# Kernel optimization log

Hardware: AMD Instinct MI355X
Metric: run time of the kernel (lower is better)

Reference implementation:

```python
import jax, jax.numpy as jnp
import numpy as np

STEPS, K, NEW_PTS, GDIM, HDIM = 10, 64, 1152, 256, 128


def setup_inputs() -> dict:
    key = jax.random.key(0)
    ks = jax.random.split(key, 24)
    def w(k, shape):
        return jax.random.normal(k, shape, dtype=jnp.float32) * 0.02
    inp = {
        'points': jax.random.normal(ks[0], (4, 4096, 3), dtype=jnp.float32),
        'gt': jax.random.normal(ks[1], (4, 4096, 3), dtype=jnp.float32),
        # PointNet encoder: 3->64->128->256 (stored [in,out])
        'enc_w1': w(ks[2], (3, 64)),   'enc_b1': jnp.zeros((64,), jnp.float32),
        'enc_w2': w(ks[3], (64, 128)), 'enc_b2': jnp.zeros((128,), jnp.float32),
        'enc_w3': w(ks[4], (128, GDIM)), 'enc_b3': jnp.zeros((GDIM,), jnp.float32),
        # Attention MLP: (3+256+128)->128->1
        'att_w1': w(ks[5], (3 + GDIM + HDIM, 128)), 'att_b1': jnp.zeros((128,), jnp.float32),
        'att_w2': w(ks[6], (128, 1)), 'att_b2': jnp.zeros((1,), jnp.float32),
        # LSTMCell: input 256+3+3=262, hidden 128, gates i,f,g,o
        'lstm_wih': w(ks[7], (GDIM + 6, 4 * HDIM)), 'lstm_whh': w(ks[8], (HDIM, 4 * HDIM)),
        'lstm_bih': jnp.zeros((4 * HDIM,), jnp.float32), 'lstm_bhh': jnp.zeros((4 * HDIM,), jnp.float32),
        # Refiner: 128->128->new_points*3
        'ref_w1': w(ks[9], (HDIM, 128)), 'ref_b1': jnp.zeros((128,), jnp.float32),
        'ref_w2': w(ks[10], (128, NEW_PTS * 3)), 'ref_b2': jnp.zeros((NEW_PTS * 3,), jnp.float32),
    }
    return inp


def _chamfer_sq(x, y):
    # x: [B,N,3], y: [B,M,3]; squared-L2 chamfer, batch-mean (pytorch3d norm=2)
    d2 = (jnp.sum(x * x, -1)[:, :, None] + jnp.sum(y * y, -1)[:, None, :]
          - 2.0 * jnp.einsum('bnd,bmd->bnm', x, y))  # [B,N,M]
    cd = jnp.mean(jnp.min(d2, axis=2), axis=1) + jnp.mean(jnp.min(d2, axis=1), axis=1)
    return jnp.mean(cd)


def _forward(points, gt, enc_w1, enc_b1, enc_w2, enc_b2, enc_w3, enc_b3,
             att_w1, att_b1, att_w2, att_b2,
             lstm_wih, lstm_whh, lstm_bih, lstm_bhh,
             ref_w1, ref_b1, ref_w2, ref_b2):
    B, N0, _ = points.shape
    h = jnp.zeros((B, HDIM), points.dtype)
    c = jnp.zeros((B, HDIM), points.dtype)
    canvas = points
    for _ in range(STEPS):
        # PointNet encoder + max-pool -> global feature [B,GDIM]
        f = jax.nn.relu(canvas @ enc_w1 + enc_b1)
        f = jax.nn.relu(f @ enc_w2 + enc_b2)
        f = f @ enc_w3 + enc_b3
        gfeat = jnp.max(f, axis=1)
        # attention-weighted centroid
        N = canvas.shape[1]
        ctx = jnp.concatenate([
            canvas,
            jnp.broadcast_to(gfeat[:, None, :], (B, N, GDIM)),
            jnp.broadcast_to(h[:, None, :], (B, N, HDIM)),
        ], axis=-1)
        scores = (jax.nn.relu(ctx @ att_w1 + att_b1) @ att_w2 + att_b2)[..., 0]  # [B,N]
        alpha = jax.nn.softmax(scores, axis=1)
        center = jnp.einsum('bn,bnd->bd', alpha, canvas)
        # brute-force KNN around center + gather
        dist = jnp.linalg.norm(canvas - center[:, None, :], axis=-1)  # [B,N]
        _, idx = jax.lax.top_k(-dist, K)  # smallest K
        patch = jnp.take_along_axis(canvas, idx[:, :, None], axis=1)  # [B,K,3]
        patch_feat = jnp.mean(patch - center[:, None, :], axis=1)  # [B,3]
        # LSTM cell (gate order i,f,g,o)
        lstm_in = jnp.concatenate([gfeat, center, patch_feat], axis=1)
        gates = lstm_in @ lstm_wih + lstm_bih + h @ lstm_whh + lstm_bhh
        gi, gf, gg, go = jnp.split(gates, 4, axis=1)
        c = jax.nn.sigmoid(gf) * c + jax.nn.sigmoid(gi) * jnp.tanh(gg)
        h = jax.nn.sigmoid(go) * jnp.tanh(c)
        # refine: generate new patch points around center
        new_pts = (jax.nn.relu(h @ ref_w1 + ref_b1) @ ref_w2 + ref_b2)
        new_pts = new_pts.reshape(B, NEW_PTS, 3) * 0.02 + center[:, None, :]
        canvas = jnp.concatenate([canvas, new_pts], axis=1)
    p_input = canvas[:, :N0, :]
    p_new = canvas[:, N0:, :]
    total_loss = 0.1 * _chamfer_sq(p_input, gt) + 1.0 * _chamfer_sq(p_new, gt)
    return total_loss


def reference(points, gt, enc_w1, enc_b1, enc_w2, enc_b2, enc_w3, enc_b3,
              att_w1, att_b1, att_w2, att_b2,
              lstm_wih, lstm_whh, lstm_bih, lstm_bhh,
              ref_w1, ref_b1, ref_w2, ref_b2):
    return _forward(points, gt, enc_w1, enc_b1, enc_w2, enc_b2, enc_w3, enc_b3,
                    att_w1, att_b1, att_w2, att_b2,
                    lstm_wih, lstm_whh, lstm_bih, lstm_bhh,
                    ref_w1, ref_b1, ref_w2, ref_b2)
```

## Files before the change

### kernel.cpp

```cpp
#include <hip/hip_runtime.h>
#include <math.h>

#define BB 4
#define N0 4096
#define NEWP 1152
#define GD 256
#define HD 128
#define KSEL 64
#define NSTEPS 10
#define NMAX (N0 + NSTEPS*NEWP)
#define NNEW (NSTEPS*NEWP)

#define OFF_CANVAS 0
#define OFF_MINAB  (OFF_CANVAS + BB*NMAX*3)
#define OFF_MINCD  (OFF_MINAB + 2*BB*N0)
#define OFF_GMAX   (OFF_MINCD + BB*NNEW + BB*N0)
#define OFF_H      (OFF_GMAX + BB*GD)
#define OFF_C      (OFF_H + 2*BB*HD)
#define OFF_ACC    (OFF_C + 2*BB*HD)
#define OFF_CENTER (OFF_ACC + 16)
#define OFF_W2T    (OFF_CENTER + 32)
#define OFF_PART   (OFF_W2T + 128*64)
#define OFF_GPART  (OFF_PART + BB*32*8)
#define WS_FLOATS  (OFF_GPART + 32*BB*512)

__device__ __forceinline__ unsigned enc_f(float f){
  unsigned u = __float_as_uint(f);
  return (u & 0x80000000u) ? ~u : (u | 0x80000000u);
}
__device__ __forceinline__ float dec_f(unsigned e){
  unsigned u = (e & 0x80000000u) ? (e & 0x7fffffffu) : ~e;
  return __uint_as_float(u);
}
__device__ __forceinline__ float sigm(float x){ return 1.f/(1.f+expf(-x)); }

__device__ __forceinline__ float block_sum(float v, volatile float* red){
#pragma unroll
  for (int s=32;s>0;s>>=1) v += __shfl_down(v, s, 64);
  int lane = threadIdx.x & 63, w = threadIdx.x >> 6, nw = blockDim.x >> 6;
  __syncthreads();
  if (lane==0) red[w] = v;
  __syncthreads();
  if (w==0){
    float x = (lane < nw) ? red[lane] : 0.f;
#pragma unroll
    for (int s=8;s>0;s>>=1) x += __shfl_down(x, s, 64);
    if (lane==0) red[0] = x;
  }
  __syncthreads();
  float r = red[0];
  __syncthreads();
  return r;
}
__device__ __forceinline__ float block_max(float v, volatile float* red){
#pragma unroll
  for (int s=32;s>0;s>>=1) v = fmaxf(v, __shfl_down(v, s, 64));
  int lane = threadIdx.x & 63, w = threadIdx.x >> 6, nw = blockDim.x >> 6;
  __syncthreads();
  if (lane==0) red[w] = v;
  __syncthreads();
  if (w==0){
    float x = (lane < nw) ? red[lane] : -3.4e38f;
#pragma unroll
    for (int s=8;s>0;s>>=1) x = fmaxf(x, __shfl_down(x, s, 64));
    if (lane==0) red[0] = x;
  }
  __syncthreads();
  float r = red[0];
  __syncthreads();
  return r;
}

__device__ __forceinline__ void enc64(
    const float* __restrict__ sP, float* __restrict__ sF1, float* __restrict__ sF2,
    const float* __restrict__ w1, const float* __restrict__ b1,
    const float* __restrict__ w2t, const float* __restrict__ b2,
    const float* __restrict__ w3, const float* __restrict__ b3,
    unsigned* __restrict__ gmax_b)
{
  int tid = threadIdx.x;
  int lane = tid & 63;
  int wv = __builtin_amdgcn_readfirstlane(tid >> 6);
#pragma unroll
  for (int k=0;k<8;k++){
    int pt = wv + 8*k;
    float p0 = sP[pt*3], p1 = sP[pt*3+1], p2 = sP[pt*3+2];
    float v = b1[lane] + p0*w1[lane] + p1*w1[64+lane] + p2*w1[128+lane];
    sF1[pt*65 + lane] = fmaxf(v, 0.f);
  }
  __syncthreads();
#pragma unroll
  for (int k=0;k<16;k++){
    int feat = wv + 8*k;
    const float* wr = w2t + feat*64;
    float a2 = b2[feat];
#pragma unroll
    for (int kk=0;kk<64;kk++) a2 += sF1[lane*65 + kk]*wr[kk];
    sF2[lane*129 + feat] = fmaxf(a2, 0.f);
  }
  __syncthreads();
  {
    float a3[32];
    const float* b3p = b3 + wv*32;
#pragma unroll
    for (int d=0;d<32;d++) a3[d] = b3p[d];
    for (int k=0;k<128;k++){
      float fk = sF2[lane*129 + k];
      const float* wr = w3 + k*256 + wv*32;
#pragma unroll
      for (int d=0;d<32;d++) a3[d] += fk*wr[d];
    }
#pragma unroll
    for (int d=0;d<32;d++){
      float v = a3[d];
#pragma unroll
      for (int s=32;s>0;s>>=1) v = fmaxf(v, __shfl_down(v, s, 64));
      if (lane==0) atomicMax(&gmax_b[wv*32 + d], enc_f(v));
    }
  }
}

__global__ __launch_bounds__(512) void init_kernel(
    const float* __restrict__ points, const float* __restrict__ w2,
    float* __restrict__ canvas, unsigned* __restrict__ minAB,
    unsigned* __restrict__ minCD, unsigned* __restrict__ gmax,
    float* __restrict__ h, float* __restrict__ c, float* __restrict__ w2t)
{
  int gid = blockIdx.x*512 + threadIdx.x;
  if (gid < BB*N0*3){
    int b = gid/(N0*3), r = gid - b*(N0*3);
    canvas[(size_t)b*NMAX*3 + r] = points[gid];
  }
  if (gid < 2*BB*N0) minAB[gid] = 0xFFFFFFFFu;
  if (gid < BB*NNEW + BB*N0) minCD[gid] = 0xFFFFFFFFu;
  if (gid < BB*GD) gmax[gid] = 0u;
  if (gid < 2*BB*HD){ h[gid]=0.f; c[gid]=0.f; }
  if (gid < 128*64){ int j=gid>>6, k=gid&63; w2t[gid] = w2[k*128+j]; }
}

__global__ __launch_bounds__(512) void enc_kernel(
    const float* __restrict__ canvas,
    const float* __restrict__ w1, const float* __restrict__ b1,
    const float* __restrict__ w2t, const float* __restrict__ b2,
    const float* __restrict__ w3, const float* __restrict__ b3,
    unsigned* __restrict__ gmax)
{
  __shared__ float sP[192], sF1[64*65], sF2[64*129];
  int b = blockIdx.y, lg = blockIdx.x;
  int tid = threadIdx.x;
  if (tid < 192) sP[tid] = canvas[(size_t)b*NMAX*3 + (size_t)lg*192 + tid];
  __syncthreads();
  enc64(sP, sF1, sF2, w1, b1, w2t, b2, w3, b3, gmax + b*GD);
}

__global__ __launch_bounds__(512) void sl_kernel(
    const float* __restrict__ canvas, const float* __restrict__ aw1,
    const float* __restrict__ ab1, const float* __restrict__ aw2,
    const float* __restrict__ ab2, const unsigned* __restrict__ gmax,
    const float* __restrict__ h_in,
    const float* __restrict__ wih, const float* __restrict__ whh,
    float* __restrict__ part, float* __restrict__ gpart, int N, int nch)
{
  __shared__ float sBatt[128];
  __shared__ float red[16];
  __shared__ float sV[BB][12];
  int blk = blockIdx.x;
  int tid = threadIdx.x;
  if (blk < 4*nch){
    int b = blk / nch, ch = blk - b*nch;
    if (tid < 128){
      float a = ab1[tid];
      for (int k=0;k<GD;k++) a += dec_f(gmax[b*GD+k]) * aw1[(3+k)*128 + tid];
      for (int k=0;k<HD;k++) a += h_in[b*HD+k] * aw1[(3+GD+k)*128 + tid];
      sBatt[tid] = a;
    }
    __syncthreads();
    int i = ch*512 + tid;
    bool act = i < N;
    float p0=0.f,p1=0.f,p2=0.f,s=-3.4e38f;
    if (act){
      const float* pp = canvas + (size_t)(b*NMAX + i)*3;
      p0=pp[0]; p1=pp[1]; p2=pp[2];
      s = ab2[0];
      for (int j=0;j<128;j++){
        float v = sBatt[j] + p0*aw1[j] + p1*aw1[128+j] + p2*aw1[256+j];
        s += fmaxf(v, 0.f)*aw2[j];
      }
    }
    float mb = block_max(s, red);
    float e = act ? expf(s - mb) : 0.f;
    float se = block_sum(e, red);
    float wx = block_sum(e*p0, red);
    float wy = block_sum(e*p1, red);
    float wz = block_sum(e*p2, red);
    if (tid==0){
      float* pr = part + (size_t)(b*32 + ch)*8;
      pr[0]=mb; pr[1]=se; pr[2]=wx; pr[3]=wy; pr[4]=wz;
    }
  } else {
    int cc = blk - 4*nch;
    if (tid < BB*12){
      int b = tid/12, j = tid - b*12;
      int r = cc*12 + j;
      sV[b][j] = (r < 256) ? dec_f(gmax[b*GD + r]) : h_in[b*HD + (r-256)];
    }
    __syncthreads();
    float a0=0.f,a1=0.f,a2=0.f,a3=0.f;
#pragma unroll
    for (int j=0;j<12;j++){
      int r = cc*12 + j;
      const float* wr = (r < 256) ? (wih + (size_t)r*512) : (whh + (size_t)(r-256)*512);
      float wvv = wr[tid];
      a0 += sV[0][j]*wvv; a1 += sV[1][j]*wvv;
      a2 += sV[2][j]*wvv; a3 += sV[3][j]*wvv;
    }
    float* gp = gpart + (size_t)cc*(BB*512);
    gp[0*512+tid]=a0; gp[1*512+tid]=a1; gp[2*512+tid]=a2; gp[3*512+tid]=a3;
  }
}

__global__ __launch_bounds__(1024) void stepA_kernel(
    const float* __restrict__ canvas, const float* __restrict__ part,
    float* __restrict__ centerpf, int N, int nch)
{
  __shared__ float red[16];
  __shared__ float sC[3];
  __shared__ unsigned cbufA[2][16];
  __shared__ unsigned cbufB[2][16];
  __shared__ int tieCnt;
  __shared__ int tieIdx[256];

  int b = blockIdx.x;
  int tid = threadIdx.x;
  int lane = tid & 63, wid = tid >> 6;
  const float* cv = canvas + (size_t)b*NMAX*3;

  float pm=-3.4e38f, pse=0.f, pwx=0.f, pwy=0.f, pwz=0.f;
  if (tid < nch){
    const float* pp = part + (size_t)(b*32 + tid)*8;
    pm=pp[0]; pse=pp[1]; pwx=pp[2]; pwy=pp[3]; pwz=pp[4];
  }
  float M = block_max(pm, red);
  float w = (tid < nch) ? expf(pm - M) : 0.f;
  float se = block_sum(pse*w, red);
  float wx = block_sum(pwx*w, red);
  float wy = block_sum(pwy*w, red);
  float wz = block_sum(pwz*w, red);
  if (tid==0){ sC[0]=wx/se; sC[1]=wy/se; sC[2]=wz/se; }
  __syncthreads();
  float cx=sC[0], cy=sC[1], cz=sC[2];
  if (tid<3) centerpf[b*3+tid] = sC[tid];

  unsigned ur[16];
#pragma unroll
  for (int q=0;q<16;q++){
    ur[q] = 0xFFFFFFFFu;
    int i = tid + q*1024;
    if (i < N){
      const float* p = cv + (size_t)i*3;
      float dx=p[0]-cx, dy=p[1]-cy, dz=p[2]-cz;
      ur[q] = __float_as_uint(dx*dx + dy*dy + dz*dz);
    }
  }

  unsigned T = 0u;
  int cntBelow = 0;
  int par = 0;
  {
    unsigned cand = 1u<<30;
    unsigned tc = 0;
#pragma unroll
    for (int q=0;q<16;q++) tc += (ur[q] < cand) ? 1u : 0u;
#pragma unroll
    for (int s=32;s>0;s>>=1) tc += __shfl_down(tc, s, 64);
    if (lane==0) cbufA[par][wid] = tc;
    __syncthreads();
    unsigned tot = 0;
#pragma unroll
    for (int i2=0;i2<16;i2++) tot += cbufA[par][i2];
    if ((int)tot < KSEL){ T = cand; cntBelow = (int)tot; }
    par ^= 1;
  }
  for (int bit=29; bit>=1; bit-=2){
    unsigned q1 = 1u<<(bit-1);
    unsigned c1 = T + q1, c2 = T + 2u*q1, c3 = T + 3u*q1;
    unsigned ta = 0, tb = 0;
#pragma unroll
    for (int q=0;q<16;q++){
      unsigned u = ur[q];
      ta += (u < c1 ? 1u : 0u) | (u < c2 ? 0x10000u : 0u);
      tb += (u < c3 ? 1u : 0u);
    }
#pragma unroll
    for (int s=32;s>0;s>>=1){ ta += __shfl_down(ta, s, 64); tb += __shfl_down(tb, s, 64); }
    if (lane==0){ cbufA[par][wid] = ta; cbufB[par][wid] = tb; }
    __syncthreads();
    unsigned sa = 0, sb = 0;
#pragma unroll
    for (int i2=0;i2<16;i2++){ sa += cbufA[par][i2]; sb += cbufB[par][i2]; }
    int n1 = (int)(sa & 0xFFFFu), n2 = (int)(sa >> 16), n3 = (int)sb;
    if (n3 < KSEL){ T = c3; cntBelow = n3; }
    else if (n2 < KSEL){ T = c2; cntBelow = n2; }
    else if (n1 < KSEL){ T = c1; cntBelow = n1; }
    par ^= 1;
  }
  int kneed = KSEL - cntBelow;

  if (tid==0) tieCnt = 0;
  __syncthreads();
  float sx=0.f, sy=0.f, sz=0.f;
#pragma unroll
  for (int q=0;q<16;q++){
    unsigned u = ur[q];
    if (u < T){
      const float* p = cv + (size_t)(tid + q*1024)*3;
      sx += p[0]; sy += p[1]; sz += p[2];
    } else if (u == T){
      int pos = atomicAdd(&tieCnt, 1);
      if (pos < 256) tieIdx[pos] = tid + q*1024;
    }
  }
  __syncthreads();
  sx = block_sum(sx, red);
  sy = block_sum(sy, red);
  sz = block_sum(sz, red);
  if (tid==0){
    int mm = tieCnt < 256 ? tieCnt : 256;
    for (int t=0;t<kneed;t++){
      int best=-1, bi=0x7fffffff;
      for (int q=0;q<mm;q++){ int v = tieIdx[q]; if (v < bi){ bi=v; best=q; } }
      if (best >= 0){
        tieIdx[best] = 0x7fffffff;
        const float* p = cv + (size_t)bi*3;
        sx += p[0]; sy += p[1]; sz += p[2];
      }
    }
    centerpf[16 + b*3 + 0] = sx/KSEL - cx;
    centerpf[16 + b*3 + 1] = sy/KSEL - cy;
    centerpf[16 + b*3 + 2] = sz/KSEL - cz;
  }
}

__global__ __launch_bounds__(512) void refine_enc_kernel(
    float* __restrict__ canvas, const float* __restrict__ gpart,
    const float* __restrict__ centerpf,
    const float* __restrict__ c_in, float* __restrict__ c_out,
    float* __restrict__ h_out,
    const float* __restrict__ wih,
    const float* __restrict__ bih, const float* __restrict__ bhh,
    const float* __restrict__ rw1, const float* __restrict__ rb1,
    const float* __restrict__ rw2, const float* __restrict__ rb2,
    const float* __restrict__ w1, const float* __restrict__ b1,
    const float* __restrict__ w2t, const float* __restrict__ b2,
    const float* __restrict__ w3, const float* __restrict__ b3,
    unsigned* __restrict__ gmax, int N)
{
  __shared__ float sG[512];
  __shared__ float sH[HD];
  __shared__ float sRf[HD];
  __shared__ float sP[192];
  __shared__ float sF1[64*65], sF2[64*129];
  int g = blockIdx.x, b = blockIdx.y;
  int tid = threadIdx.x;
  float cx = centerpf[b*3+0], cy = centerpf[b*3+1], cz = centerpf[b*3+2];
  float fx = centerpf[16+b*3+0], fy = centerpf[16+b*3+1], fz = centerpf[16+b*3+2];
  {
    float gg = bih[tid] + bhh[tid];
    for (int cc=0; cc<32; cc++) gg += gpart[(size_t)cc*(BB*512) + b*512 + tid];
    gg += cx*wih[(size_t)256*512+tid] + cy*wih[(size_t)257*512+tid] + cz*wih[(size_t)258*512+tid];
    gg += fx*wih[(size_t)259*512+tid] + fy*wih[(size_t)260*512+tid] + fz*wih[(size_t)261*512+tid];
    sG[tid] = gg;
  }
  __syncthreads();
  if (tid < HD){
    float gi=sG[tid], gf=sG[128+tid], gg2=sG[256+tid], go=sG[384+tid];
    float cn = sigm(gf)*c_in[b*HD+tid] + sigm(gi)*tanhf(gg2);
    float hn = sigm(go)*tanhf(cn);
    sH[tid] = hn;
    if (g==0){ c_out[b*HD+tid]=cn; h_out[b*HD+tid]=hn; }
  }
  __syncthreads();
  if (tid < HD){
    float a = rb1[tid];
    for (int k=0;k<HD;k++) a += sH[k]*rw1[k*HD + tid];
    sRf[tid] = fmaxf(a, 0.f);
  }
  __syncthreads();
  if (tid < 192){
    int o = g*192 + tid;
    float a = rb2[o];
    for (int k=0;k<HD;k++) a += sRf[k]*rw2[(size_t)k*(NEWP*3) + o];
    float val = a*0.02f + centerpf[b*3 + (tid%3)];
    sP[tid] = val;
    canvas[((size_t)b*NMAX + N)*3 + o] = val;
  }
  __syncthreads();
  enc64(sP, sF1, sF2, w1, b1, w2t, b2, w3, b3, gmax + b*GD);
}

__global__ __launch_bounds__(512) void chamfer_kernel(
    const float* __restrict__ canvas, const float* __restrict__ gt,
    unsigned* __restrict__ minAB, unsigned* __restrict__ minCD)
{
  __shared__ float sy0[1024], sy1[1024], sy2[1024], sny[1024];
  int id = blockIdx.x;
  int dir, rem;
  if (id < 32){ dir=0; rem=id; }
  else if (id < 64){ dir=1; rem=id-32; }
  else if (id < 160){ dir=2; rem=id-64; }
  else { dir=3; rem=id-160; }
  int b, xb, yb;
  if (dir < 2){ b = rem>>3; int l = rem&7; xb = l>>2; yb = l&3; }
  else if (dir == 2){ b = rem/24; int l = rem%24; xb = l>>2; yb = l&3; }
  else { b = rem/24; int l = rem%24; xb = l/12; yb = l%12; }

  int Nx, Ny; const float* X; const float* Y; unsigned* mp;
  if (dir==0){      Nx=N0;   Ny=N0;   X=canvas+(size_t)b*NMAX*3;       Y=gt+(size_t)b*N0*3;            mp=minAB + b*N0; }
  else if (dir==1){ Nx=N0;   Ny=N0;   X=gt+(size_t)b*N0*3;             Y=canvas+(size_t)b*NMAX*3;      mp=minAB + BB*N0 + b*N0; }
  else if (dir==2){ Nx=NNEW; Ny=N0;   X=canvas+((size_t)b*NMAX+N0)*3;  Y=gt+(size_t)b*N0*3;            mp=minCD + b*NNEW; }
  else {            Nx=N0;   Ny=NNEW; X=gt+(size_t)b*N0*3;             Y=canvas+((size_t)b*NMAX+N0)*3; mp=minCD + BB*NNEW + b*N0; }

  int xbase = xb*2048;
  int ybase = yb*1024;
  int tn = min(1024, Ny - ybase);
  int tid = threadIdx.x;
  for (int t=tid; t<tn; t+=512){
    const float* yp = Y + (size_t)(ybase+t)*3;
    float y0=yp[0], y1=yp[1], y2=yp[2];
    sy0[t]=y0; sy1[t]=y1; sy2[t]=y2; sny[t]=y0*y0+y1*y1+y2*y2;
  }
  __syncthreads();

  float X0[4],X1[4],X2[4],NXr[4],MN[4]; int XI[4]; bool VA[4];
#pragma unroll
  for (int q=0;q<4;q++){
    int x = xbase + q*512 + tid;
    VA[q] = x < Nx;
    int xc = VA[q] ? x : 0;
    const float* xp = X + (size_t)xc*3;
    X0[q]=xp[0]; X1[q]=xp[1]; X2[q]=xp[2];
    NXr[q] = X0[q]*X0[q] + X1[q]*X1[q] + X2[q]*X2[q];
    MN[q] = 3.4e38f; XI[q] = xc;
  }
  const float4* v0 = (const float4*)sy0;
  const float4* v1 = (const float4*)sy1;
  const float4* v2 = (const float4*)sy2;
  const float4* vn = (const float4*)sny;
  int j4n = tn >> 2;
  for (int j=0;j<j4n;j++){
    float4 a0 = v0[j], a1 = v1[j], a2 = v2[j], an = vn[j];
#pragma unroll
    for (int e=0;e<4;e++){
      float y0 = ((const float*)&a0)[e];
      float y1 = ((const float*)&a1)[e];
      float y2 = ((const float*)&a2)[e];
      float ny = ((const float*)&an)[e];
#pragma unroll
      for (int q=0;q<4;q++){
        float dot = fmaf(X0[q], y0, fmaf(X1[q], y1, X2[q]*y2));
        MN[q] = fminf(MN[q], fmaf(-2.f, dot, ny));
      }
    }
  }
  for (int j=j4n*4; j<tn; j++){
    float y0=sy0[j], y1=sy1[j], y2=sy2[j], ny=sny[j];
#pragma unroll
    for (int q=0;q<4;q++){
      float dot = fmaf(X0[q], y0, fmaf(X1[q], y1, X2[q]*y2));
      MN[q] = fminf(MN[q], fmaf(-2.f, dot, ny));
    }
  }
#pragma unroll
  for (int q=0;q<4;q++)
    if (VA[q]) atomicMin(&mp[XI[q]], enc_f(MN[q] + NXr[q]));
}

__global__ __launch_bounds__(256) void chamfer_reduce_kernel(
    const unsigned* __restrict__ minAB, const unsigned* __restrict__ minCD,
    float* __restrict__ acc)
{
  __shared__ float red[16];
  int s = blockIdx.x, dir = s>>2, b = s&3;
  const unsigned* mp; int len;
  if (dir==0){      mp=minAB + b*N0;            len=N0; }
  else if (dir==1){ mp=minAB + BB*N0 + b*N0;    len=N0; }
  else if (dir==2){ mp=minCD + b*NNEW;          len=NNEW; }
  else {            mp=minCD + BB*NNEW + b*N0;  len=N0; }
  float v = 0.f;
  for (int i=threadIdx.x;i<len;i+=256) v += dec_f(mp[i]);
  v = block_sum(v, red);
  if (threadIdx.x==0) acc[s] = v;
}

__global__ void finish_kernel(const float* __restrict__ acc, float* __restrict__ out)
{
  if (threadIdx.x == 0 && blockIdx.x == 0){
    float cd1 = 0.f, cd2 = 0.f;
    for (int b=0;b<BB;b++) cd1 += acc[b]/(float)N0 + acc[4+b]/(float)N0;
    for (int b=0;b<BB;b++) cd2 += acc[8+b]/(float)NNEW + acc[12+b]/(float)N0;
    out[0] = 0.1f*(cd1/BB) + 1.0f*(cd2/BB);
  }
}

extern "C" void kernel_launch(void* const* d_in, const int* in_sizes, int n_in,
                              void* d_out, int out_size, void* d_ws, size_t ws_size,
                              hipStream_t stream) {
  (void)in_sizes; (void)n_in; (void)out_size; (void)ws_size;
  const float* points   = (const float*)d_in[0];
  const float* gt       = (const float*)d_in[1];
  const float* enc_w1   = (const float*)d_in[2];
  const float* enc_b1   = (const float*)d_in[3];
  const float* enc_w2   = (const float*)d_in[4];
  const float* enc_b2   = (const float*)d_in[5];
  const float* enc_w3   = (const float*)d_in[6];
  const float* enc_b3   = (const float*)d_in[7];
  const float* att_w1   = (const float*)d_in[8];
  const float* att_b1   = (const float*)d_in[9];
  const float* att_w2   = (const float*)d_in[10];
  const float* att_b2   = (const float*)d_in[11];
  const float* lstm_wih = (const float*)d_in[12];
  const float* lstm_whh = (const float*)d_in[13];
  const float* lstm_bih = (const float*)d_in[14];
  const float* lstm_bhh = (const float*)d_in[15];
  const float* ref_w1   = (const float*)d_in[16];
  const float* ref_b1   = (const float*)d_in[17];
  const float* ref_w2   = (const float*)d_in[18];
  const float* ref_b2   = (const float*)d_in[19];
  float* out = (float*)d_out;

  float* ws       = (float*)d_ws;
  float* canvas   = ws + OFF_CANVAS;
  unsigned* minAB = (unsigned*)(ws + OFF_MINAB);
  unsigned* minCD = (unsigned*)(ws + OFF_MINCD);
  unsigned* gmaxp = (unsigned*)(ws + OFF_GMAX);
  float* hb       = ws + OFF_H;
  float* cb       = ws + OFF_C;
  float* acc      = ws + OFF_ACC;
  float* centerb  = ws + OFF_CENTER;
  float* w2t      = ws + OFF_W2T;
  float* partb    = ws + OFF_PART;
  float* gpartb   = ws + OFF_GPART;

  init_kernel<<<dim3(128), 512, 0, stream>>>(points, enc_w2, canvas, minAB, minCD, gmaxp, hb, cb, w2t);
  enc_kernel<<<dim3(64, BB), 512, 0, stream>>>(canvas, enc_w1, enc_b1, w2t, enc_b2, enc_w3, enc_b3, gmaxp);

  for (int t=0; t<NSTEPS; t++){
    int N   = N0 + t*NEWP;
    int nch = (N + 511) >> 9;
    float* h_in  = hb + (t&1)*BB*HD;
    float* h_out = hb + ((t+1)&1)*BB*HD;
    float* c_in  = cb + (t&1)*BB*HD;
    float* c_out = cb + ((t+1)&1)*BB*HD;
    sl_kernel<<<dim3(4*nch + 32), 512, 0, stream>>>(canvas, att_w1, att_b1, att_w2, att_b2,
                                                    gmaxp, h_in, lstm_wih, lstm_whh,
                                                    partb, gpartb, N, nch);
    stepA_kernel<<<dim3(BB), 1024, 0, stream>>>(canvas, partb, centerb, N, nch);
    refine_enc_kernel<<<dim3(18, BB), 512, 0, stream>>>(canvas, gpartb, centerb,
                                                        c_in, c_out, h_out,
                                                        lstm_wih, lstm_bih, lstm_bhh,
                                                        ref_w1, ref_b1, ref_w2, ref_b2,
                                                        enc_w1, enc_b1, w2t, enc_b2, enc_w3, enc_b3,
                                                        gmaxp, N);
  }

  chamfer_kernel<<<dim3(256), 512, 0, stream>>>(canvas, gt, minAB, minCD);
  chamfer_reduce_kernel<<<dim3(16), 256, 0, stream>>>(minAB, minCD, acc);
  finish_kernel<<<1, 64, 0, stream>>>(acc, out);
}
```

Before: 1.139 ms.

## Split PointNet encoder into separate point-parallel layer kernels via global buffer

Replaces the fused per-64-point shared-memory encoder with two kernels. One computes layers 1-2 per point into a global feature buffer, and the other computes layer 3 with the max-pool. Both spread work over output-channel chunks along the grid z dimension. The encoder is also taken out of the refine kernel, which now only produces new points with 256-thread blocks. This gives more parallel blocks and lowers register and LDS pressure, at the cost of two extra launches per step and a global-memory round trip for the 128-channel intermediate. Layer 1 is recomputed in each channel chunk.

```diff
diff --git a/kernel.cpp b/kernel.cpp
--- a/kernel.cpp
+++ b/kernel.cpp
@@ -10,6 +10,7 @@
 #define NSTEPS 10
 #define NMAX (N0 + NSTEPS*NEWP)
 #define NNEW (NSTEPS*NEWP)
+#define F2S (BB*N0)
 
 #define OFF_CANVAS 0
 #define OFF_MINAB  (OFF_CANVAS + BB*NMAX*3)
@@ -19,10 +20,10 @@
 #define OFF_C      (OFF_H + 2*BB*HD)
 #define OFF_ACC    (OFF_C + 2*BB*HD)
 #define OFF_CENTER (OFF_ACC + 16)
-#define OFF_W2T    (OFF_CENTER + 32)
-#define OFF_PART   (OFF_W2T + 128*64)
+#define OFF_PART   (OFF_CENTER + 32)
 #define OFF_GPART  (OFF_PART + BB*32*8)
-#define WS_FLOATS  (OFF_GPART + 32*BB*512)
+#define OFF_F2     (OFF_GPART + 32*BB*512)
+#define WS_FLOATS  (OFF_F2 + 128*F2S)
 
 __device__ __forceinline__ unsigned enc_f(float f){
   unsigned u = __float_as_uint(f);
@@ -71,60 +72,11 @@
   return r;
 }
 
-__device__ __forceinline__ void enc64(
-    const float* __restrict__ sP, float* __restrict__ sF1, float* __restrict__ sF2,
-    const float* __restrict__ w1, const float* __restrict__ b1,
-    const float* __restrict__ w2t, const float* __restrict__ b2,
-    const float* __restrict__ w3, const float* __restrict__ b3,
-    unsigned* __restrict__ gmax_b)
-{
-  int tid = threadIdx.x;
-  int lane = tid & 63;
-  int wv = __builtin_amdgcn_readfirstlane(tid >> 6);
-#pragma unroll
-  for (int k=0;k<8;k++){
-    int pt = wv + 8*k;
-    float p0 = sP[pt*3], p1 = sP[pt*3+1], p2 = sP[pt*3+2];
-    float v = b1[lane] + p0*w1[lane] + p1*w1[64+lane] + p2*w1[128+lane];
-    sF1[pt*65 + lane] = fmaxf(v, 0.f);
-  }
-  __syncthreads();
-#pragma unroll
-  for (int k=0;k<16;k++){
-    int feat = wv + 8*k;
-    const float* wr = w2t + feat*64;
-    float a2 = b2[feat];
-#pragma unroll
-    for (int kk=0;kk<64;kk++) a2 += sF1[lane*65 + kk]*wr[kk];
-    sF2[lane*129 + feat] = fmaxf(a2, 0.f);
-  }
-  __syncthreads();
-  {
-    float a3[32];
-    const float* b3p = b3 + wv*32;
-#pragma unroll
-    for (int d=0;d<32;d++) a3[d] = b3p[d];
-    for (int k=0;k<128;k++){
-      float fk = sF2[lane*129 + k];
-      const float* wr = w3 + k*256 + wv*32;
-#pragma unroll
-      for (int d=0;d<32;d++) a3[d] += fk*wr[d];
-    }
-#pragma unroll
-    for (int d=0;d<32;d++){
-      float v = a3[d];
-#pragma unroll
-      for (int s=32;s>0;s>>=1) v = fmaxf(v, __shfl_down(v, s, 64));
-      if (lane==0) atomicMax(&gmax_b[wv*32 + d], enc_f(v));
-    }
-  }
-}
-
 __global__ __launch_bounds__(512) void init_kernel(
-    const float* __restrict__ points, const float* __restrict__ w2,
+    const float* __restrict__ points,
     float* __restrict__ canvas, unsigned* __restrict__ minAB,
     unsigned* __restrict__ minCD, unsigned* __restrict__ gmax,
-    float* __restrict__ h, float* __restrict__ c, float* __restrict__ w2t)
+    float* __restrict__ h, float* __restrict__ c)
 {
   int gid = blockIdx.x*512 + threadIdx.x;
   if (gid < BB*N0*3){
@@ -135,22 +87,69 @@
   if (gid < BB*NNEW + BB*N0) minCD[gid] = 0xFFFFFFFFu;
   if (gid < BB*GD) gmax[gid] = 0u;
   if (gid < 2*BB*HD){ h[gid]=0.f; c[gid]=0.f; }
-  if (gid < 128*64){ int j=gid>>6, k=gid&63; w2t[gid] = w2[k*128+j]; }
-}
-
-__global__ __launch_bounds__(512) void enc_kernel(
-    const float* __restrict__ canvas,
-    const float* __restrict__ w1, const float* __restrict__ b1,
-    const float* __restrict__ w2t, const float* __restrict__ b2,
-    const float* __restrict__ w3, const float* __restrict__ b3,
-    unsigned* __restrict__ gmax)
-{
-  __shared__ float sP[192], sF1[64*65], sF2[64*129];
-  int b = blockIdx.y, lg = blockIdx.x;
-  int tid = threadIdx.x;
-  if (tid < 192) sP[tid] = canvas[(size_t)b*NMAX*3 + (size_t)lg*192 + tid];
-  __syncthreads();
-  enc64(sP, sF1, sF2, w1, b1, w2t, b2, w3, b3, gmax + b*GD);
+}
+
+__global__ __launch_bounds__(256) void enc12_kernel(
+    const float* __restrict__ canvas, const float* __restrict__ w1,
+    const float* __restrict__ b1, const float* __restrict__ w2,
+    const float* __restrict__ b2, float* __restrict__ f2buf,
+    int off, int M)
+{
+  int b = blockIdx.y;
+  int jc = blockIdx.z;
+  int i = blockIdx.x*256 + threadIdx.x;
+  int ii = (i < M) ? i : 0;
+  const float* p = canvas + (size_t)(b*NMAX + off + ii)*3;
+  float p0 = p[0], p1 = p[1], p2 = p[2];
+  float f1[64];
+#pragma unroll
+  for (int j=0;j<64;j++)
+    f1[j] = fmaxf(0.f, b1[j] + p0*w1[j] + p1*w1[64+j] + p2*w1[128+j]);
+  float a[16];
+  const float* b2p = b2 + jc*16;
+#pragma unroll
+  for (int j=0;j<16;j++) a[j] = b2p[j];
+#pragma unroll
+  for (int k=0;k<64;k++){
+    const float* wr = w2 + k*128 + jc*16;
+#pragma unroll
+    for (int j=0;j<16;j++) a[j] = fmaf(f1[k], wr[j], a[j]);
+  }
+  if (i < M){
+    int base = b*N0 + i;
+#pragma unroll
+    for (int j=0;j<16;j++)
+      f2buf[(size_t)(jc*16 + j)*F2S + base] = fmaxf(a[j], 0.f);
+  }
+}
+
+__global__ __launch_bounds__(256) void enc3_kernel(
+    const float* __restrict__ f2buf, const float* __restrict__ w3,
+    const float* __restrict__ b3, unsigned* __restrict__ gmax, int M)
+{
+  int b = blockIdx.y;
+  int dc = blockIdx.z;
+  int i = blockIdx.x*256 + threadIdx.x;
+  bool act = i < M;
+  int ii = act ? i : 0;
+  const float* fp = f2buf + b*N0 + ii;
+  float a[16];
+  const float* b3p = b3 + dc*16;
+#pragma unroll
+  for (int d=0;d<16;d++) a[d] = b3p[d];
+  for (int k=0;k<128;k++){
+    float fk = fp[(size_t)k*F2S];
+    const float* wr = w3 + k*256 + dc*16;
+#pragma unroll
+    for (int d=0;d<16;d++) a[d] = fmaf(fk, wr[d], a[d]);
+  }
+#pragma unroll
+  for (int d=0;d<16;d++){
+    float v = act ? a[d] : -3.4e38f;
+#pragma unroll
+    for (int s=32;s>0;s>>=1) v = fmaxf(v, __shfl_down(v, s, 64));
+    if ((threadIdx.x & 63) == 0) atomicMax(&gmax[b*GD + dc*16 + d], enc_f(v));
+  }
 }
 
 __global__ __launch_bounds__(512) void sl_kernel(
@@ -341,7 +340,7 @@
   }
 }
 
-__global__ __launch_bounds__(512) void refine_enc_kernel(
+__global__ __launch_bounds__(256) void refine_kernel(
     float* __restrict__ canvas, const float* __restrict__ gpart,
     const float* __restrict__ centerpf,
     const float* __restrict__ c_in, float* __restrict__ c_out,
@@ -349,27 +348,23 @@
     const float* __restrict__ wih,
     const float* __restrict__ bih, const float* __restrict__ bhh,
     const float* __restrict__ rw1, const float* __restrict__ rb1,
-    const float* __restrict__ rw2, const float* __restrict__ rb2,
-    const float* __restrict__ w1, const float* __restrict__ b1,
-    const float* __restrict__ w2t, const float* __restrict__ b2,
-    const float* __restrict__ w3, const float* __restrict__ b3,
-    unsigned* __restrict__ gmax, int N)
+    const float* __restrict__ rw2, const float* __restrict__ rb2, int N)
 {
   __shared__ float sG[512];
   __shared__ float sH[HD];
   __shared__ float sRf[HD];
-  __shared__ float sP[192];
-  __shared__ float sF1[64*65], sF2[64*129];
   int g = blockIdx.x, b = blockIdx.y;
   int tid = threadIdx.x;
   float cx = centerpf[b*3+0], cy = centerpf[b*3+1], cz = centerpf[b*3+2];
   float fx = centerpf[16+b*3+0], fy = centerpf[16+b*3+1], fz = centerpf[16+b*3+2];
-  {
-    float gg = bih[tid] + bhh[tid];
-    for (int cc=0; cc<32; cc++) gg += gpart[(size_t)cc*(BB*512) + b*512 + tid];
-    gg += cx*wih[(size_t)256*512+tid] + cy*wih[(size_t)257*512+tid] + cz*wih[(size_t)258*512+tid];
-    gg += fx*wih[(size_t)259*512+tid] + fy*wih[(size_t)260*512+tid] + fz*wih[(size_t)261*512+tid];
-    sG[tid] = gg;
+#pragma unroll
+  for (int half=0; half<2; half++){
+    int o = tid + half*256;
+    float gg = bih[o] + bhh[o];
+    for (int cc=0; cc<32; cc++) gg += gpart[(size_t)cc*(BB*512) + b*512 + o];
+    gg += cx*wih[(size_t)256*512+o] + cy*wih[(size_t)257*512+o] + cz*wih[(size_t)258*512+o];
+    gg += fx*wih[(size_t)259*512+o] + fy*wih[(size_t)260*512+o] + fz*wih[(size_t)261*512+o];
+    sG[o] = gg;
   }
   __syncthreads();
   if (tid < HD){
@@ -386,16 +381,12 @@
     sRf[tid] = fmaxf(a, 0.f);
   }
   __syncthreads();
-  if (tid < 192){
-    int o = g*192 + tid;
+  int o = g*256 + tid;
+  if (o < NEWP*3){
     float a = rb2[o];
     for (int k=0;k<HD;k++) a += sRf[k]*rw2[(size_t)k*(NEWP*3) + o];
-    float val = a*0.02f + centerpf[b*3 + (tid%3)];
-    sP[tid] = val;
-    canvas[((size_t)b*NMAX + N)*3 + o] = val;
-  }
-  __syncthreads();
-  enc64(sP, sF1, sF2, w1, b1, w2t, b2, w3, b3, gmax + b*GD);
+    canvas[((size_t)b*NMAX + N)*3 + o] = a*0.02f + centerpf[b*3 + (o%3)];
+  }
 }
 
 __global__ __launch_bounds__(512) void chamfer_kernel(
@@ -537,12 +528,13 @@
   float* cb       = ws + OFF_C;
   float* acc      = ws + OFF_ACC;
   float* centerb  = ws + OFF_CENTER;
-  float* w2t      = ws + OFF_W2T;
   float* partb    = ws + OFF_PART;
   float* gpartb   = ws + OFF_GPART;
-
-  init_kernel<<<dim3(128), 512, 0, stream>>>(points, enc_w2, canvas, minAB, minCD, gmaxp, hb, cb, w2t);
-  enc_kernel<<<dim3(64, BB), 512, 0, stream>>>(canvas, enc_w1, enc_b1, w2t, enc_b2, enc_w3, enc_b3, gmaxp);
+  float* f2buf    = ws + OFF_F2;
+
+  init_kernel<<<dim3(128), 512, 0, stream>>>(points, canvas, minAB, minCD, gmaxp, hb, cb);
+  enc12_kernel<<<dim3(16, BB, 8), 256, 0, stream>>>(canvas, enc_w1, enc_b1, enc_w2, enc_b2, f2buf, 0, N0);
+  enc3_kernel<<<dim3(16, BB, 16), 256, 0, stream>>>(f2buf, enc_w3, enc_b3, gmaxp, N0);
 
   for (int t=0; t<NSTEPS; t++){
     int N   = N0 + t*NEWP;
@@ -555,12 +547,12 @@
                                                     gmaxp, h_in, lstm_wih, lstm_whh,
                                                     partb, gpartb, N, nch);
     stepA_kernel<<<dim3(BB), 1024, 0, stream>>>(canvas, partb, centerb, N, nch);
-    refine_enc_kernel<<<dim3(18, BB), 512, 0, stream>>>(canvas, gpartb, centerb,
-                                                        c_in, c_out, h_out,
-                                                        lstm_wih, lstm_bih, lstm_bhh,
-                                                        ref_w1, ref_b1, ref_w2, ref_b2,
-                                                        enc_w1, enc_b1, w2t, enc_b2, enc_w3, enc_b3,
-                                                        gmaxp, N);
+    refine_kernel<<<dim3(14, BB), 256, 0, stream>>>(canvas, gpartb, centerb,
+                                                    c_in, c_out, h_out,
+                                                    lstm_wih, lstm_bih, lstm_bhh,
+                                                    ref_w1, ref_b1, ref_w2, ref_b2, N);
+    enc12_kernel<<<dim3(5, BB, 8), 256, 0, stream>>>(canvas, enc_w1, enc_b1, enc_w2, enc_b2, f2buf, N, NEWP);
+    enc3_kernel<<<dim3(5, BB, 16), 256, 0, stream>>>(f2buf, enc_w3, enc_b3, gmaxp, NEWP);
   }
 
   chamfer_kernel<<<dim3(256), 512, 0, stream>>>(canvas, gt, minAB, minCD);
```

After: 1.089 ms. 4.4% less time.
